# Optimization experiments

Measured on AMD Instinct MI355X. Metric: run time of the kernel, lower is better.

Reference implementation:

```python
import jax, jax.numpy as jnp
import numpy as np

B, T, O = 32, 2048, 18            # batch, triples per graph, hardcoded object count
DIN1, H, DOUT = 1500, 512, 512    # net1 input dim is hardcoded 1500 in the source

def _kaiming(key, fan_in, fan_out):
    return jax.random.normal(key, (fan_in, fan_out), jnp.float32) * np.sqrt(2.0 / fan_in)

def setup_inputs() -> dict:
    key = jax.random.key(0)
    ks = jax.random.split(key, 8)
    trip = jax.random.normal(ks[0], (B, T, DIN1), jnp.float32)
    index = jax.random.randint(ks[1], (B, T, 2), 0, O)
    rel_lens = jax.random.randint(ks[2], (B,), 0, T)
    # net1: 1500 -> H -> 2H+Dout (ReLU after every layer incl. last)
    w1a = _kaiming(ks[3], DIN1, H); b1a = jnp.zeros((H,), jnp.float32)
    w1b = _kaiming(ks[4], H, 2 * H + DOUT); b1b = jnp.zeros((2 * H + DOUT,), jnp.float32)
    # net2: H -> H -> Dout (ReLU after every layer incl. last)
    w2a = _kaiming(ks[5], H, H); b2a = jnp.zeros((H,), jnp.float32)
    w2b = _kaiming(ks[6], H, DOUT); b2b = jnp.zeros((DOUT,), jnp.float32)
    return dict(trip=trip, index=index, rel_lens=rel_lens,
                w1a=w1a, b1a=b1a, w1b=w1b, b1b=b1b,
                w2a=w2a, b2a=b2a, w2b=w2b, b2b=b2b)

def reference(trip, index, rel_lens, w1a, b1a, w1b, b1b, w2a, b2a, w2b, b2b):
    # net1 MLP over all triples: [B,T,1500] -> [B,T,2H+Dout]
    h = jax.nn.relu(trip @ w1a + b1a)
    new_t = jax.nn.relu(h @ w1b + b1b)
    s_vecs = new_t[..., :H]              # [B,T,H] subject
    p_vecs = new_t[..., H:H + DOUT]      # [B,T,Dout] predicate (returned as-is)
    o_vecs = new_t[..., H + DOUT:]       # [B,T,H] object
    # mask out triples beyond rel_lens[i]
    mask = (jnp.arange(T)[None, :] < rel_lens[:, None]).astype(new_t.dtype)  # [B,T]
    oh_s = jax.nn.one_hot(index[..., 0], O, dtype=new_t.dtype) * mask[..., None]  # [B,T,O]
    oh_o = jax.nn.one_hot(index[..., 1], O, dtype=new_t.dtype) * mask[..., None]
    # per-batch scatter_add pooling into the O=18 object slots
    contrib = (jnp.einsum('bto,bth->boh', oh_s, s_vecs)
               + jnp.einsum('bto,bth->boh', oh_o, o_vecs))  # [B,O,H]
    # original code never resets pooled_obj_vecs inside the batch loop ->
    # accumulation is CUMULATIVE over batch items
    pooled = jnp.cumsum(contrib, axis=0)  # [B,O,H]
    # net2 MLP on each cumulative pool
    h2 = jax.nn.relu(pooled @ w2a + b2a)
    new_obj = jax.nn.relu(h2 @ w2b + b2b)  # [B,O,Dout]
    return new_obj, p_vecs
```

## Files before the change

### kernel.cpp

```cpp
#include <hip/hip_runtime.h>
#include <hip/hip_bf16.h>

#define NBATCH 32
#define NTIME  2048
#define NOBJ   18
#define KIN    1500
#define NH     512
#define NTOT   1536
#define NM     65536

typedef __attribute__((ext_vector_type(4))) float f32x4;
typedef __attribute__((ext_vector_type(8))) short s16x8;
typedef __attribute__((ext_vector_type(4))) short s16x4;

static __device__ __forceinline__ short f2bf(float f) {
  union { float f; unsigned u; } v; v.f = f;
  unsigned r = v.u + 0x7fffu + ((v.u >> 16) & 1u);
  return (short)(r >> 16);
}

static __device__ __forceinline__ void gload_lds16(const short* g, short* l) {
  __builtin_amdgcn_global_load_lds(
      (const __attribute__((address_space(1))) unsigned int*)(g),
      (__attribute__((address_space(3))) unsigned int*)(l), 16, 0, 0);
}

__global__ void k_prep(const float* __restrict__ src, short* __restrict__ dst,
                       int K, int Nsrc, int nkt, int total) {
  int i = blockIdx.x * 256 + threadIdx.x;
  if (i >= total) return;
  int chunk = i >> 14, off = i & 16383;
  int row = off >> 6, kcp = off & 63;
  int kc = kcp ^ ((row & 7) << 3);
  int cb = chunk / nkt, kt = chunk - cb * nkt;
  int n = cb * 256 + row, k = kt * 64 + kc;
  dst[i] = (k < K) ? f2bf(src[(size_t)k * Nsrc + n]) : (short)0;
}

__launch_bounds__(512, 2)
__global__ void k_gemm1(const float* __restrict__ A, const short* __restrict__ Bc,
                        const float* __restrict__ bias, short* __restrict__ Hc) {
  __shared__ short lA[2][256 * 64];
  __shared__ short lB[2][256 * 64];
  const int g = blockIdx.x;
  const int lid = (g & 7) * 64 + (g >> 3);
  const int rb = lid >> 1, cb = lid & 1;
  const int m0 = rb * 256, n0 = cb * 256;
  const int tid = threadIdx.x;
  const int lane = tid & 63, w = tid >> 6;
  const int wr = w >> 2, wc = w & 3;
  const int rlane = lane & 15, ksel = (lane >> 4) * 8;
  const int swz = (rlane & 7) << 3;
  const int kx0 = ksel ^ swz, kx1 = (32 | ksel) ^ swz;
  const int arow = tid >> 4;
  const int akq  = (tid & 15) * 4;
  const short* bchunk = Bc + (size_t)(cb * 24) * 16384;

  f32x4 acc[8][4] = {};
  float4 av[8];
  s16x8 af[4][2];
  s16x8 bfr[2][2];

  auto issueA = [&](int kt) {
    const int kbase = kt * 64;
    const bool fullq = (kt < 23) | (akq <= 24);
#pragma unroll
    for (int i = 0; i < 8; ++i) {
      const float* p = A + (size_t)(m0 + arow + i * 32) * KIN + kbase + akq;
      av[i] = fullq ? *(const float4*)p : make_float4(0.f, 0.f, 0.f, 0.f);
    }
  };
  auto writeA = [&](int nb) {
#pragma unroll
    for (int i = 0; i < 8; ++i) {
      int r = arow + i * 32;
      s16x4 h4;
      h4[0] = f2bf(av[i].x); h4[1] = f2bf(av[i].y);
      h4[2] = f2bf(av[i].z); h4[3] = f2bf(av[i].w);
      *(s16x4*)&lA[nb][r * 64 + (akq ^ ((r & 7) << 3))] = h4;
    }
  };
  auto issueB = [&](int nb, int kt, int h) {
    const short* src = bchunk + (size_t)kt * 16384 + h * 8192 + tid * 8;
#pragma unroll
    for (int j = 0; j < 2; ++j)
      gload_lds16(src + j * 4096, &lB[nb][h * 8192 + tid * 8 + j * 4096]);
  };
  auto readA = [&](int cu, int rh) {
#pragma unroll
    for (int mm = 0; mm < 4; ++mm) {
      int ro = (rh * 128 + wr * 64 + mm * 16 + rlane) * 64;
      af[mm][0] = *(const s16x8*)&lA[cu][ro + kx0];
      af[mm][1] = *(const s16x8*)&lA[cu][ro + kx1];
    }
  };
  auto readB = [&](int cu, int ch) {
#pragma unroll
    for (int qn = 0; qn < 2; ++qn) {
      int ro = (ch * 128 + wc * 32 + qn * 16 + rlane) * 64;
      bfr[qn][0] = *(const s16x8*)&lB[cu][ro + kx0];
      bfr[qn][1] = *(const s16x8*)&lB[cu][ro + kx1];
    }
  };
  auto mfma_quad = [&](int rh, int ch) {
    __builtin_amdgcn_s_setprio(1);
#pragma unroll
    for (int j = 0; j < 2; ++j)
#pragma unroll
      for (int mm = 0; mm < 4; ++mm)
#pragma unroll
        for (int qn = 0; qn < 2; ++qn)
          acc[rh * 4 + mm][ch * 2 + qn] = __builtin_amdgcn_mfma_f32_16x16x32_bf16(
              af[mm][j], bfr[qn][j], acc[rh * 4 + mm][ch * 2 + qn], 0, 0, 0);
    __builtin_amdgcn_s_setprio(0);
  };

  issueA(0);
  issueB(0, 0, 0);
  issueB(0, 0, 1);
  writeA(0);
  asm volatile("s_waitcnt lgkmcnt(0)" ::: "memory");

#define G1_TILE(KT, W0S, W1S, HASNEXT)                                  \
  {                                                                     \
    const int cu = (KT) & 1, nb = cu ^ 1;                               \
    asm volatile("s_waitcnt vmcnt(" W0S ")" ::: "memory");              \
    __builtin_amdgcn_s_barrier();                                       \
    asm volatile("" ::: "memory");                                      \
    if (HASNEXT) issueA((KT) + 1);                                      \
    readA(cu, 0); readB(cu, 0);                                         \
    mfma_quad(0, 0);                                                    \
    asm volatile("s_waitcnt vmcnt(" W1S ")" ::: "memory");              \
    __builtin_amdgcn_s_barrier();                                       \
    asm volatile("" ::: "memory");                                      \
    if (HASNEXT) issueB(nb, (KT) + 1, 0);                               \
    readB(cu, 1);                                                       \
    mfma_quad(0, 1);                                                    \
    __builtin_amdgcn_s_barrier();                                       \
    asm volatile("" ::: "memory");                                      \
    if (HASNEXT) issueB(nb, (KT) + 1, 1);                               \
    readA(cu, 1);                                                       \
    mfma_quad(1, 1);                                                    \
    __builtin_amdgcn_s_barrier();                                       \
    asm volatile("" ::: "memory");                                      \
    if (HASNEXT) writeA(nb);                                            \
    readB(cu, 0);                                                       \
    mfma_quad(1, 0);                                                    \
    if (HASNEXT) asm volatile("s_waitcnt lgkmcnt(0)" ::: "memory");     \
  }

#pragma unroll 1
  for (int kt = 0; kt < 23; ++kt) G1_TILE(kt, "2", "8", 1);
  G1_TILE(23, "2", "0", 0);
#undef G1_TILE

#pragma unroll
  for (int n = 0; n < 4; ++n) {
    int c = n0 + (n >> 1) * 128 + wc * 32 + (n & 1) * 16 + rlane;
    float bv = bias[c];
#pragma unroll
    for (int m = 0; m < 8; ++m) {
      int rbase = m0 + (m >> 2) * 128 + wr * 64 + (m & 3) * 16 + ((lane >> 4) << 2);
#pragma unroll
      for (int q = 0; q < 4; ++q) {
        int r = rbase + q;
        float v = acc[m][n][q] + bv;
        v = v > 0.f ? v : 0.f;
        Hc[(size_t)(((r >> 8) * 8 + (c >> 6)) * 16384) + (r & 255) * 64 +
           ((c & 63) ^ ((r & 7) << 3))] = f2bf(v);
      }
    }
  }
}

__launch_bounds__(512, 2)
__global__ void k_gemm2(const short* __restrict__ Ac, const short* __restrict__ Bc,
                        const float* __restrict__ bias, const int* __restrict__ index,
                        const int* __restrict__ rel_lens,
                        float* __restrict__ contrib, float* __restrict__ out) {
  __shared__ short lA[2][256 * 64];
  __shared__ short lB[2][256 * 64];
  const int g = blockIdx.x;
  const int lid = (g & 7) * 192 + (g >> 3);
  const int rb = lid / 6, cb = lid - rb * 6;
  const int m0 = rb * 256;
  const int tid = threadIdx.x;
  const int lane = tid & 63, w = tid >> 6;
  const int wr = w >> 2, wc = w & 3;
  const int rlane = lane & 15, ksel = (lane >> 4) * 8;
  const int swz = (rlane & 7) << 3;
  const int kx0 = ksel ^ swz, kx1 = (32 | ksel) ^ swz;
  const short* achunk = Ac + (size_t)(rb * 8) * 16384;
  const short* bchunk = Bc + (size_t)(cb * 8) * 16384;

  f32x4 acc[8][4] = {};
  s16x8 af[4][2], bf0[2][2], bf1[2][2];

  auto issueA = [&](int nb, int kt, int h) {
    const short* src = achunk + (size_t)kt * 16384 + h * 8192 + tid * 8;
#pragma unroll
    for (int j = 0; j < 2; ++j)
      gload_lds16(src + j * 4096, &lA[nb][h * 8192 + tid * 8 + j * 4096]);
  };
  auto issueB = [&](int nb, int kt, int h) {
    const short* src = bchunk + (size_t)kt * 16384 + h * 8192 + tid * 8;
#pragma unroll
    for (int j = 0; j < 2; ++j)
      gload_lds16(src + j * 4096, &lB[nb][h * 8192 + tid * 8 + j * 4096]);
  };
  auto readA = [&](int cu, int rh) {
#pragma unroll
    for (int mm = 0; mm < 4; ++mm) {
      int ro = (rh * 128 + wr * 64 + mm * 16 + rlane) * 64;
      af[mm][0] = *(const s16x8*)&lA[cu][ro + kx0];
      af[mm][1] = *(const s16x8*)&lA[cu][ro + kx1];
    }
  };
  auto readB = [&](int cu, int ch, s16x8 (&dst)[2][2]) {
#pragma unroll
    for (int qn = 0; qn < 2; ++qn) {
      int ro = (ch * 128 + wc * 32 + qn * 16 + rlane) * 64;
      dst[qn][0] = *(const s16x8*)&lB[cu][ro + kx0];
      dst[qn][1] = *(const s16x8*)&lB[cu][ro + kx1];
    }
  };
  auto mfma_quad = [&](int rh, int ch, s16x8 (&bfr)[2][2]) {
    __builtin_amdgcn_s_setprio(1);
#pragma unroll
    for (int j = 0; j < 2; ++j)
#pragma unroll
      for (int mm = 0; mm < 4; ++mm)
#pragma unroll
        for (int qn = 0; qn < 2; ++qn)
          acc[rh * 4 + mm][ch * 2 + qn] = __builtin_amdgcn_mfma_f32_16x16x32_bf16(
              af[mm][j], bfr[qn][j], acc[rh * 4 + mm][ch * 2 + qn], 0, 0, 0);
    __builtin_amdgcn_s_setprio(0);
  };

  issueA(0, 0, 0);
  issueB(0, 0, 0);
  issueB(0, 0, 1);
  issueA(0, 0, 1);

#define G2_TILE(KT, W0S, W1S, W2S, HASNEXT)                             \
  {                                                                     \
    const int cu = (KT) & 1, nb = cu ^ 1;                               \
    asm volatile("s_waitcnt vmcnt(" W0S ")" ::: "memory");              \
    __builtin_amdgcn_s_barrier();                                       \
    asm volatile("" ::: "memory");                                      \
    if (HASNEXT) issueA(nb, (KT) + 1, 0);                               \
    readA(cu, 0); readB(cu, 0, bf0);                                    \
    mfma_quad(0, 0, bf0);                                               \
    asm volatile("s_waitcnt vmcnt(" W1S ")" ::: "memory");              \
    __builtin_amdgcn_s_barrier();                                       \
    asm volatile("" ::: "memory");                                      \
    if (HASNEXT) issueB(nb, (KT) + 1, 0);                               \
    readB(cu, 1, bf1);                                                  \
    mfma_quad(0, 1, bf1);                                               \
    asm volatile("s_waitcnt vmcnt(" W2S ")" ::: "memory");              \
    __builtin_amdgcn_s_barrier();                                       \
    asm volatile("" ::: "memory");                                      \
    if (HASNEXT) issueB(nb, (KT) + 1, 1);                               \
    readA(cu, 1);                                                       \
    mfma_quad(1, 1, bf1);                                               \
    __builtin_amdgcn_s_barrier();                                       \
    asm volatile("" ::: "memory");                                      \
    if (HASNEXT) issueA(nb, (KT) + 1, 1);                               \
    mfma_quad(1, 0, bf0);                                               \
  }

#pragma unroll 1
  for (int kt = 0; kt < 7; ++kt) G2_TILE(kt, "4", "4", "4", 1);
  G2_TILE(7, "4", "2", "0", 0);
#undef G2_TILE

  const int region = cb >> 1;
  float bv[4]; int cg[4];
#pragma unroll
  for (int n = 0; n < 4; ++n) {
    cg[n] = cb * 256 + (n >> 1) * 128 + wc * 32 + (n & 1) * 16 + rlane;
    bv[n] = bias[cg[n]];
  }

  if (region == 1) {
    float* po = out + (size_t)NBATCH * NOBJ * NH;
#pragma unroll
    for (int m = 0; m < 8; ++m) {
      int rbase = m0 + (m >> 2) * 128 + wr * 64 + (m & 3) * 16 + ((lane >> 4) << 2);
#pragma unroll
      for (int q = 0; q < 4; ++q) {
#pragma unroll
        for (int n = 0; n < 4; ++n) {
          float v = acc[m][n][q] + bv[n];
          v = v > 0.f ? v : 0.f;
          po[(size_t)(rbase + q) * NH + (cg[n] & 511)] = v;
        }
      }
    }
  } else {
    const int sel = region >> 1;
    const int b = m0 >> 11;
    const int rel = rel_lens[b];
#pragma unroll
    for (int m = 0; m < 8; ++m) {
      int rbase = m0 + (m >> 2) * 128 + wr * 64 + (m & 3) * 16 + ((lane >> 4) << 2);
#pragma unroll
      for (int q = 0; q < 4; ++q) {
        int r = rbase + q;
        if ((r & 2047) < rel) {
          int idx = index[2 * r + sel];
          float* dst = contrib + ((b * NOBJ + idx) << 9);
#pragma unroll
          for (int n = 0; n < 4; ++n) {
            float v = acc[m][n][q] + bv[n];
            v = v > 0.f ? v : 0.f;
            atomicAdd(dst + (cg[n] & 511), v);
          }
        }
      }
    }
  }
}

__global__ void k_cumsum(const float* __restrict__ contrib, float* __restrict__ pooled) {
  int i = blockIdx.x * 256 + threadIdx.x;
  if (i >= NOBJ * NH) return;
  float a = 0.f;
#pragma unroll
  for (int b = 0; b < NBATCH; ++b) {
    a += contrib[b * (NOBJ * NH) + i];
    pooled[b * (NOBJ * NH) + i] = a;
  }
}

__global__ void k_mlp2(const float* __restrict__ pooled,
                       const float* __restrict__ w2a, const float* __restrict__ b2a,
                       const float* __restrict__ w2b, const float* __restrict__ b2b,
                       float* __restrict__ out) {
  __shared__ float pr[NH];
  __shared__ float hr[NH];
  int row = blockIdx.x;
  int tid = threadIdx.x;
  pr[tid]       = pooled[(size_t)row * NH + tid];
  pr[tid + 256] = pooled[(size_t)row * NH + tid + 256];
  __syncthreads();
  float s0 = 0.f, s1 = 0.f;
  for (int k = 0; k < NH; ++k) {
    float p = pr[k];
    s0 += p * w2a[k * NH + tid];
    s1 += p * w2a[k * NH + tid + 256];
  }
  s0 += b2a[tid]; s1 += b2a[tid + 256];
  hr[tid]       = s0 > 0.f ? s0 : 0.f;
  hr[tid + 256] = s1 > 0.f ? s1 : 0.f;
  __syncthreads();
  s0 = 0.f; s1 = 0.f;
  for (int k = 0; k < NH; ++k) {
    float h = hr[k];
    s0 += h * w2b[k * NH + tid];
    s1 += h * w2b[k * NH + tid + 256];
  }
  s0 += b2b[tid]; s1 += b2b[tid + 256];
  out[(size_t)row * NH + tid]       = s0 > 0.f ? s0 : 0.f;
  out[(size_t)row * NH + tid + 256] = s1 > 0.f ? s1 : 0.f;
}

extern "C" void kernel_launch(void* const* d_in, const int* in_sizes, int n_in,
                              void* d_out, int out_size, void* d_ws, size_t ws_size,
                              hipStream_t stream) {
  const float* trip     = (const float*)d_in[0];
  const int*   index    = (const int*)d_in[1];
  const int*   rel_lens = (const int*)d_in[2];
  const float* w1a      = (const float*)d_in[3];
  const float* b1a      = (const float*)d_in[4];
  const float* w1b      = (const float*)d_in[5];
  const float* b1b      = (const float*)d_in[6];
  const float* w2a      = (const float*)d_in[7];
  const float* b2a      = (const float*)d_in[8];
  const float* w2b      = (const float*)d_in[9];
  const float* b2b      = (const float*)d_in[10];
  float* out = (float*)d_out;

  char* ws = (char*)d_ws;
  short* wt1a    = (short*)(ws);
  short* wt1b    = (short*)(ws + 1572864);
  short* hbuf    = (short*)(ws + 3145728);
  float* contrib = (float*)(ws + 70254592);
  float* pooled  = contrib + NBATCH * NOBJ * NH;

  k_prep<<<3072, 256, 0, stream>>>(w1a, wt1a, KIN, NH, 24, NH * 1536);
  k_prep<<<3072, 256, 0, stream>>>(w1b, wt1b, NH, NTOT, 8, NTOT * NH);
  hipMemsetAsync(contrib, 0, (size_t)NBATCH * NOBJ * NH * sizeof(float), stream);
  k_gemm1<<<512, 512, 0, stream>>>(trip, wt1a, b1a, hbuf);
  k_gemm2<<<1536, 512, 0, stream>>>(hbuf, wt1b, b1b, index, rel_lens, contrib, out);
  k_cumsum<<<36, 256, 0, stream>>>(contrib, pooled);
  k_mlp2<<<576, 256, 0, stream>>>(pooled, w2a, b2a, w2b, b2b, out);
}
```

Baseline: 471.8 us.

## Restructure GEMM main loops into ping-pong barrier schedule with split A prefetch

Rewrites the software pipeline in both GEMM kernels so each MFMA quadrant is bracketed by barriers. LDS fragment reads and global prefetches for the next tile are issued before the barrier, in the style of a ping-pong schedule. In gemm1 the A-tile fp32 loads are split into two halves, which halves the staging registers and spreads the bf16 conversion and LDS writes across the iteration. It also replaces hipMemsetAsync with a small zero-fill kernel. The extra barriers add synchronisation cost and could stall waves if the overlap does not materialise.

```diff
diff --git a/kernel.cpp b/kernel.cpp
--- a/kernel.cpp
+++ b/kernel.cpp
@@ -24,6 +24,10 @@
       (const __attribute__((address_space(1))) unsigned int*)(g),
       (__attribute__((address_space(3))) unsigned int*)(l), 16, 0, 0);
 }
+
+#define FENCE() asm volatile("" ::: "memory")
+#define BAR()   do { FENCE(); __builtin_amdgcn_s_barrier(); FENCE(); } while (0)
+#define LGKM0() asm volatile("s_waitcnt lgkmcnt(0)" ::: "memory")
 
 __global__ void k_prep(const float* __restrict__ src, short* __restrict__ dst,
                        int K, int Nsrc, int nkt, int total) {
@@ -35,6 +39,11 @@
   int cb = chunk / nkt, kt = chunk - cb * nkt;
   int n = cb * 256 + row, k = kt * 64 + kc;
   dst[i] = (k < K) ? f2bf(src[(size_t)k * Nsrc + n]) : (short)0;
+}
+
+__global__ void k_zero(float* __restrict__ p, int n) {
+  int i = blockIdx.x * 256 + threadIdx.x;
+  if (i < n) p[i] = 0.f;
 }
 
 __launch_bounds__(512, 2)
@@ -57,23 +66,23 @@
   const short* bchunk = Bc + (size_t)(cb * 24) * 16384;
 
   f32x4 acc[8][4] = {};
-  float4 av[8];
+  float4 av[4];
   s16x8 af[4][2];
-  s16x8 bfr[2][2];
-
-  auto issueA = [&](int kt) {
+  s16x8 bf0[2][2], bf1[2][2];
+
+  auto issueA_h = [&](int kt, int h) {
     const int kbase = kt * 64;
     const bool fullq = (kt < 23) | (akq <= 24);
 #pragma unroll
-    for (int i = 0; i < 8; ++i) {
-      const float* p = A + (size_t)(m0 + arow + i * 32) * KIN + kbase + akq;
+    for (int i = 0; i < 4; ++i) {
+      const float* p = A + (size_t)(m0 + arow + (h * 4 + i) * 32) * KIN + kbase + akq;
       av[i] = fullq ? *(const float4*)p : make_float4(0.f, 0.f, 0.f, 0.f);
     }
   };
-  auto writeA = [&](int nb) {
-#pragma unroll
-    for (int i = 0; i < 8; ++i) {
-      int r = arow + i * 32;
+  auto writeA_h = [&](int nb, int h) {
+#pragma unroll
+    for (int i = 0; i < 4; ++i) {
+      int r = arow + (h * 4 + i) * 32;
       s16x4 h4;
       h4[0] = f2bf(av[i].x); h4[1] = f2bf(av[i].y);
       h4[2] = f2bf(av[i].z); h4[3] = f2bf(av[i].w);
@@ -94,15 +103,15 @@
       af[mm][1] = *(const s16x8*)&lA[cu][ro + kx1];
     }
   };
-  auto readB = [&](int cu, int ch) {
+  auto readB = [&](int cu, int ch, s16x8 (&dst)[2][2]) {
 #pragma unroll
     for (int qn = 0; qn < 2; ++qn) {
       int ro = (ch * 128 + wc * 32 + qn * 16 + rlane) * 64;
-      bfr[qn][0] = *(const s16x8*)&lB[cu][ro + kx0];
-      bfr[qn][1] = *(const s16x8*)&lB[cu][ro + kx1];
-    }
-  };
-  auto mfma_quad = [&](int rh, int ch) {
+      dst[qn][0] = *(const s16x8*)&lB[cu][ro + kx0];
+      dst[qn][1] = *(const s16x8*)&lB[cu][ro + kx1];
+    }
+  };
+  auto mfma_quad = [&](int rh, int ch, s16x8 (&bfr)[2][2]) {
     __builtin_amdgcn_s_setprio(1);
 #pragma unroll
     for (int j = 0; j < 2; ++j)
@@ -115,44 +124,44 @@
     __builtin_amdgcn_s_setprio(0);
   };
 
-  issueA(0);
+  issueA_h(0, 0);
   issueB(0, 0, 0);
+  writeA_h(0, 0);
+  issueA_h(0, 1);
   issueB(0, 0, 1);
-  writeA(0);
-  asm volatile("s_waitcnt lgkmcnt(0)" ::: "memory");
-
-#define G1_TILE(KT, W0S, W1S, HASNEXT)                                  \
-  {                                                                     \
-    const int cu = (KT) & 1, nb = cu ^ 1;                               \
-    asm volatile("s_waitcnt vmcnt(" W0S ")" ::: "memory");              \
-    __builtin_amdgcn_s_barrier();                                       \
-    asm volatile("" ::: "memory");                                      \
-    if (HASNEXT) issueA((KT) + 1);                                      \
-    readA(cu, 0); readB(cu, 0);                                         \
-    mfma_quad(0, 0);                                                    \
-    asm volatile("s_waitcnt vmcnt(" W1S ")" ::: "memory");              \
-    __builtin_amdgcn_s_barrier();                                       \
-    asm volatile("" ::: "memory");                                      \
-    if (HASNEXT) issueB(nb, (KT) + 1, 0);                               \
-    readB(cu, 1);                                                       \
-    mfma_quad(0, 1);                                                    \
-    __builtin_amdgcn_s_barrier();                                       \
-    asm volatile("" ::: "memory");                                      \
-    if (HASNEXT) issueB(nb, (KT) + 1, 1);                               \
-    readA(cu, 1);                                                       \
-    mfma_quad(1, 1);                                                    \
-    __builtin_amdgcn_s_barrier();                                       \
-    asm volatile("" ::: "memory");                                      \
-    if (HASNEXT) writeA(nb);                                            \
-    readB(cu, 0);                                                       \
-    mfma_quad(1, 0);                                                    \
-    if (HASNEXT) asm volatile("s_waitcnt lgkmcnt(0)" ::: "memory");     \
-  }
+  writeA_h(0, 1);
+  issueA_h(1, 0);
+  LGKM0();
+  BAR();
 
 #pragma unroll 1
-  for (int kt = 0; kt < 23; ++kt) G1_TILE(kt, "2", "8", 1);
-  G1_TILE(23, "2", "0", 0);
-#undef G1_TILE
+  for (int kt = 0; kt < 24; ++kt) {
+    const int cu = kt & 1, nb = cu ^ 1;
+    const bool hn = kt < 23, hn2 = kt < 22;
+    readA(cu, 0); readB(cu, 0, bf0);
+    if (hn) issueB(nb, kt + 1, 0);
+    if (hn) { asm volatile("s_waitcnt vmcnt(6)" ::: "memory"); }
+    else    { asm volatile("s_waitcnt vmcnt(0)" ::: "memory"); }
+    BAR(); LGKM0();
+    mfma_quad(0, 0, bf0);
+    BAR();
+    readB(cu, 1, bf1);
+    if (hn) { writeA_h(nb, 0); issueA_h(kt + 1, 1); }
+    BAR(); LGKM0();
+    mfma_quad(0, 1, bf1);
+    BAR();
+    readA(cu, 1);
+    if (hn) issueB(nb, kt + 1, 1);
+    BAR(); LGKM0();
+    mfma_quad(1, 1, bf1);
+    BAR();
+    if (hn) writeA_h(nb, 1);
+    if (hn2) issueA_h(kt + 2, 0);
+    LGKM0();
+    BAR();
+    mfma_quad(1, 0, bf0);
+    BAR();
+  }
 
 #pragma unroll
   for (int n = 0; n < 4; ++n) {
@@ -241,38 +250,38 @@
   issueB(0, 0, 0);
   issueB(0, 0, 1);
   issueA(0, 0, 1);
-
-#define G2_TILE(KT, W0S, W1S, W2S, HASNEXT)                             \
-  {                                                                     \
-    const int cu = (KT) & 1, nb = cu ^ 1;                               \
-    asm volatile("s_waitcnt vmcnt(" W0S ")" ::: "memory");              \
-    __builtin_amdgcn_s_barrier();                                       \
-    asm volatile("" ::: "memory");                                      \
-    if (HASNEXT) issueA(nb, (KT) + 1, 0);                               \
-    readA(cu, 0); readB(cu, 0, bf0);                                    \
-    mfma_quad(0, 0, bf0);                                               \
-    asm volatile("s_waitcnt vmcnt(" W1S ")" ::: "memory");              \
-    __builtin_amdgcn_s_barrier();                                       \
-    asm volatile("" ::: "memory");                                      \
-    if (HASNEXT) issueB(nb, (KT) + 1, 0);                               \
-    readB(cu, 1, bf1);                                                  \
-    mfma_quad(0, 1, bf1);                                               \
-    asm volatile("s_waitcnt vmcnt(" W2S ")" ::: "memory");              \
-    __builtin_amdgcn_s_barrier();                                       \
-    asm volatile("" ::: "memory");                                      \
-    if (HASNEXT) issueB(nb, (KT) + 1, 1);                               \
-    readA(cu, 1);                                                       \
-    mfma_quad(1, 1, bf1);                                               \
-    __builtin_amdgcn_s_barrier();                                       \
-    asm volatile("" ::: "memory");                                      \
-    if (HASNEXT) issueA(nb, (KT) + 1, 1);                               \
-    mfma_quad(1, 0, bf0);                                               \
-  }
+  asm volatile("s_waitcnt vmcnt(4)" ::: "memory");
+  BAR();
 
 #pragma unroll 1
-  for (int kt = 0; kt < 7; ++kt) G2_TILE(kt, "4", "4", "4", 1);
-  G2_TILE(7, "4", "2", "0", 0);
-#undef G2_TILE
+  for (int kt = 0; kt < 8; ++kt) {
+    const int cu = kt & 1, nb = cu ^ 1;
+    const bool hn = kt < 7;
+    readA(cu, 0); readB(cu, 0, bf0);
+    if (hn) issueA(nb, kt + 1, 0);
+    if (hn) { asm volatile("s_waitcnt vmcnt(4)" ::: "memory"); }
+    else    { asm volatile("s_waitcnt vmcnt(2)" ::: "memory"); }
+    BAR(); LGKM0();
+    mfma_quad(0, 0, bf0);
+    BAR();
+    readB(cu, 1, bf1);
+    if (hn) issueB(nb, kt + 1, 0);
+    if (hn) { asm volatile("s_waitcnt vmcnt(4)" ::: "memory"); }
+    else    { asm volatile("s_waitcnt vmcnt(0)" ::: "memory"); }
+    BAR(); LGKM0();
+    mfma_quad(0, 1, bf1);
+    BAR();
+    readA(cu, 1);
+    if (hn) issueB(nb, kt + 1, 1);
+    BAR(); LGKM0();
+    mfma_quad(1, 1, bf1);
+    BAR();
+    if (hn) issueA(nb, kt + 1, 1);
+    if (hn) { asm volatile("s_waitcnt vmcnt(4)" ::: "memory"); }
+    BAR();
+    mfma_quad(1, 0, bf0);
+    BAR();
+  }
 
   const int region = cb >> 1;
   float bv[4]; int cg[4];
@@ -390,7 +399,7 @@
 
   k_prep<<<3072, 256, 0, stream>>>(w1a, wt1a, KIN, NH, 24, NH * 1536);
   k_prep<<<3072, 256, 0, stream>>>(w1b, wt1b, NH, NTOT, 8, NTOT * NH);
-  hipMemsetAsync(contrib, 0, (size_t)NBATCH * NOBJ * NH * sizeof(float), stream);
+  k_zero<<<1152, 256, 0, stream>>>(contrib, NBATCH * NOBJ * NH);
   k_gemm1<<<512, 512, 0, stream>>>(trip, wt1a, b1a, hbuf);
   k_gemm2<<<1536, 512, 0, stream>>>(hbuf, wt1b, b1b, index, rel_lens, contrib, out);
   k_cumsum<<<36, 256, 0, stream>>>(contrib, pooled);
```

After: 487.6 us. 1.03x slower.
